# Kernel optimization log

Measured on AMD Instinct MI355X. Metric: run time of the kernel, lower is better.

Reference implementation:

```python
import jax, jax.numpy as jnp
import numpy as np

N_NODES = 100000


def _gcn_norm(edge_index, num_nodes):
    # PyG GCNConv default: add self-loops, symmetric normalization
    row, col = edge_index[0], edge_index[1]
    loop = jnp.arange(num_nodes, dtype=edge_index.dtype)
    row = jnp.concatenate([row, loop])
    col = jnp.concatenate([col, loop])
    ones = jnp.ones(col.shape[0], dtype=jnp.float32)
    deg = jax.ops.segment_sum(ones, col, num_segments=num_nodes)
    dinv = jnp.where(deg > 0, jax.lax.rsqrt(deg), 0.0)
    norm = dinv[row] * dinv[col]  # [E + N]
    return row, col, norm


def _gcn_conv(x, W, b, row, col, norm, num_nodes):
    h = x @ W                               # [N, out] linear transform first
    msg = h[row] * norm[:, None]            # gather + edge-wise scale
    out = jax.ops.segment_sum(msg, col, num_segments=num_nodes)  # scatter-add
    return out + b


def setup_inputs() -> dict:
    key = jax.random.key(0)
    k1, k2, k3, k4 = jax.random.split(key, 4)
    E = 1600000
    x = jax.random.normal(k1, (N_NODES, 128), dtype=jnp.float32)
    edge_index = jax.random.randint(k2, (2, E), 0, N_NODES, dtype=jnp.int64)
    W1 = jax.random.normal(k3, (128, 128), dtype=jnp.float32) * (1.0 / np.sqrt(128))
    b1 = jnp.zeros((128,), dtype=jnp.float32)
    W2 = jax.random.normal(k4, (128, 64), dtype=jnp.float32) * (1.0 / np.sqrt(128))
    b2 = jnp.zeros((64,), dtype=jnp.float32)
    return {"x": x, "edge_index": edge_index, "W1": W1, "b1": b1, "W2": W2, "b2": b2}


def reference(x, edge_index, W1, b1, W2, b2):
    num_nodes = x.shape[0]
    row, col, norm = _gcn_norm(edge_index, num_nodes)
    h = _gcn_conv(x, W1, b1, row, col, norm, num_nodes)
    h = jax.nn.relu(h)
    out = _gcn_conv(h, W2, b2, row, col, norm, num_nodes)
    return out
```

## Files before the change

### kernel.cpp

```cpp
#include <hip/hip_runtime.h>
#include <hip/hip_bf16.h>

typedef unsigned short u16;
typedef short bf16x8 __attribute__((ext_vector_type(8)));
typedef float f32x4 __attribute__((ext_vector_type(4)));

__device__ __forceinline__ float bflo(unsigned u) { return __uint_as_float(u << 16); }
__device__ __forceinline__ float bfhi(unsigned u) { return __uint_as_float(u & 0xffff0000u); }
__device__ __forceinline__ u16 f2bf(float f) {
    unsigned u = __float_as_uint(f);
    return (u16)((u + 0x7fffu + ((u >> 16) & 1u)) >> 16);
}

#define CHUNK 8192
#define BN 512

__global__ __launch_bounds__(256) void hist_kernel(const int* __restrict__ cols,
                                                   unsigned* __restrict__ hist,
                                                   int E, int nbuckets) {
    __shared__ unsigned h[256];
    int t = threadIdx.x, blk = blockIdx.x;
    h[t] = 0;
    __syncthreads();
    int base = blk * CHUNK;
#pragma unroll
    for (int j = 0; j < CHUNK / 256; j++) {
        int i = base + j * 256 + t;
        if (i < E) atomicAdd(&h[((unsigned)cols[i]) >> 9], 1u);
    }
    __syncthreads();
    if (t < nbuckets) hist[blk * nbuckets + t] = h[t];
}

__global__ __launch_bounds__(256) void scanA1_kernel(unsigned* __restrict__ hist,
                                                     unsigned* __restrict__ totals,
                                                     int nblocksA, int nbuckets) {
    __shared__ unsigned s[256];
    int t = threadIdx.x, b = blockIdx.x;
    unsigned val = (t < nblocksA) ? hist[t * nbuckets + b] : 0u;
    s[t] = val;
    __syncthreads();
    for (int off = 1; off < 256; off <<= 1) {
        unsigned v = (t >= off) ? s[t - off] : 0u;
        __syncthreads();
        s[t] += v;
        __syncthreads();
    }
    if (t < nblocksA) hist[t * nbuckets + b] = s[t] - val;
    if (t == 255) totals[b] = s[255];
}

__global__ __launch_bounds__(256) void scanA2_kernel(const unsigned* __restrict__ totals,
                                                     unsigned* __restrict__ bucketbase,
                                                     int nbuckets) {
    __shared__ unsigned s[256];
    int t = threadIdx.x;
    unsigned val = (t < nbuckets) ? totals[t] : 0u;
    s[t] = val;
    __syncthreads();
    for (int off = 1; off < 256; off <<= 1) {
        unsigned v = (t >= off) ? s[t - off] : 0u;
        __syncthreads();
        s[t] += v;
        __syncthreads();
    }
    unsigned ex = s[t] - val;
    if (t < nbuckets) bucketbase[t] = ex;
    if (t == nbuckets - 1) bucketbase[nbuckets] = ex + val;
}

__global__ __launch_bounds__(256) void scatterA_kernel(const int* __restrict__ rows,
                                                       const int* __restrict__ cols,
                                                       const unsigned* __restrict__ hist,
                                                       const unsigned* __restrict__ bucketbase,
                                                       uint2* __restrict__ binned,
                                                       int E, int nbuckets) {
    __shared__ uint2 sp[CHUNK];
    __shared__ unsigned lstart[256];
    __shared__ unsigned lcur[256];
    __shared__ unsigned gbase[256];
    int t = threadIdx.x, blk = blockIdx.x;
    int base = blk * CHUNK;
    int cnt = min(CHUNK, E - base);

    lcur[t] = 0;
    __syncthreads();
    for (int i = t; i < cnt; i += 256)
        atomicAdd(&lcur[((unsigned)cols[base + i]) >> 9], 1u);
    __syncthreads();
    unsigned val = lcur[t];
    lstart[t] = val;
    __syncthreads();
    for (int off = 1; off < 256; off <<= 1) {
        unsigned v = (t >= off) ? lstart[t - off] : 0u;
        __syncthreads();
        lstart[t] += v;
        __syncthreads();
    }
    unsigned ex = lstart[t] - val;
    __syncthreads();
    lstart[t] = ex;
    lcur[t] = ex;
    if (t < nbuckets) gbase[t] = bucketbase[t] + hist[blk * nbuckets + t];
    __syncthreads();
    for (int i = t; i < cnt; i += 256) {
        unsigned c = (unsigned)cols[base + i];
        unsigned r = (unsigned)rows[base + i];
        unsigned pos = atomicAdd(&lcur[c >> 9], 1u);
        sp[pos] = make_uint2(r, c);
    }
    __syncthreads();
    for (int i = t; i < cnt; i += 256) {
        uint2 u = sp[i];
        unsigned g = u.y >> 9;
        binned[gbase[g] + (unsigned)i - lstart[g]] = u;
    }
}

__global__ __launch_bounds__(256) void binB_kernel(const uint2* __restrict__ binned,
                                                   const unsigned* __restrict__ bucketbase,
                                                   int* __restrict__ rowptr,
                                                   float* __restrict__ dinv,
                                                   int* __restrict__ srcidx,
                                                   int N, int E, int nbuckets) {
    __shared__ unsigned cnt[BN + 1];
    __shared__ unsigned sc[BN + 1];
    __shared__ unsigned ps[256];
    int t = threadIdx.x, b = blockIdx.x;
    int lo = b << 9;
    int nn = min(BN, N - lo);
    unsigned s = bucketbase[b], e = bucketbase[b + 1];

    cnt[t] = 0;
    cnt[t + 256] = 0;
    if (t == 0) cnt[BN] = 0;
    __syncthreads();
    for (unsigned i = s + t; i < e; i += 256)
        atomicAdd(&cnt[binned[i].y - lo], 1u);
    __syncthreads();

    unsigned a0 = cnt[2 * t], a1 = cnt[2 * t + 1];
    ps[t] = a0 + a1;
    __syncthreads();
    unsigned val = ps[t];
    for (int off = 1; off < 256; off <<= 1) {
        unsigned v = (t >= off) ? ps[t - off] : 0u;
        __syncthreads();
        ps[t] += v;
        __syncthreads();
    }
    unsigned ex = ps[t] - val;
    sc[2 * t] = ex;
    sc[2 * t + 1] = ex + a0;
    if (t == 255) sc[BN] = ex + val;
    __syncthreads();

    for (int n = t; n < nn; n += 256) {
        unsigned rp = s + sc[n];
        rowptr[lo + n] = (int)rp;
        dinv[lo + n] = rsqrtf((float)(sc[n + 1] - sc[n]) + 1.0f);
        cnt[n] = rp;
    }
    if (b == nbuckets - 1 && t == 0) rowptr[N] = E;
    __syncthreads();

    for (unsigned i = s + t; i < e; i += 256) {
        uint2 u = binned[i];
        unsigned slot = atomicAdd(&cnt[u.y - lo], 1u);
        srcidx[slot] = (int)u.x;
    }
}

__global__ __launch_bounds__(256) void prep_wt(const float* __restrict__ W1,
                                               const float* __restrict__ W2,
                                               u16* __restrict__ WT1,
                                               u16* __restrict__ WT2) {
    int t = blockIdx.x * 256 + threadIdx.x;
    if (t < 128 * 128) {
        int n = t >> 7, k = t & 127;
        WT1[n * 128 + k] = f2bf(W1[k * 128 + n]);
    } else if (t < 128 * 128 + 64 * 128) {
        int i = t - 128 * 128;
        int n = i >> 7, k = i & 127;
        WT2[n * 128 + k] = f2bf(W2[k * 64 + n]);
    }
}

template <int NOUT, bool IN_BF16>
__global__ __launch_bounds__(256) void gemm_mfma(const void* __restrict__ Xv,
                                                 const u16* __restrict__ WT,
                                                 const float* __restrict__ dinv,
                                                 u16* __restrict__ OutH, int nrows) {
    constexpr int LDK = 136;
    __shared__ u16 sX[64 * LDK];
    __shared__ u16 sW[NOUT * LDK];

    const int t = threadIdx.x;
    const int wv = t >> 6, lane = t & 63;
    const int m = lane & 15, q = lane >> 4;
    const int row0 = blockIdx.x * 64;

    for (int idx = t; idx < NOUT * 16; idx += 256) {
        int n = idx >> 4, c = idx & 15;
        *((uint4*)&sW[n * LDK + c * 8]) = ((const uint4*)WT)[idx];
    }
    if (IN_BF16) {
        const u16* X = (const u16*)Xv;
        for (int idx = t; idx < 64 * 16; idx += 256) {
            int r = idx >> 4, c = idx & 15;
            int gr = row0 + r;
            uint4 v = make_uint4(0u, 0u, 0u, 0u);
            if (gr < nrows) v = ((const uint4*)X)[(size_t)gr * 16 + c];
            *((uint4*)&sX[r * LDK + c * 8]) = v;
        }
    } else {
        const float* X = (const float*)Xv;
        for (int idx = t; idx < 64 * 32; idx += 256) {
            int r = idx >> 5, c = idx & 31;
            int gr = row0 + r;
            float4 v = make_float4(0.f, 0.f, 0.f, 0.f);
            if (gr < nrows) v = ((const float4*)X)[(size_t)gr * 32 + c];
            uint2 o;
            o.x = (unsigned)f2bf(v.x) | ((unsigned)f2bf(v.y) << 16);
            o.y = (unsigned)f2bf(v.z) | ((unsigned)f2bf(v.w) << 16);
            *((uint2*)&sX[r * LDK + c * 4]) = o;
        }
    }
    __syncthreads();

    f32x4 acc[NOUT / 16];
#pragma unroll
    for (int i = 0; i < NOUT / 16; i++) acc[i] = (f32x4){0.f, 0.f, 0.f, 0.f};

#pragma unroll
    for (int ks = 0; ks < 4; ks++) {
        const int k0 = ks * 32 + q * 8;
        bf16x8 a = *((const bf16x8*)&sX[(wv * 16 + m) * LDK + k0]);
#pragma unroll
        for (int nt = 0; nt < NOUT / 16; nt++) {
            bf16x8 b = *((const bf16x8*)&sW[(nt * 16 + m) * LDK + k0]);
            acc[nt] = __builtin_amdgcn_mfma_f32_16x16x32_bf16(a, b, acc[nt], 0, 0, 0);
        }
    }

#pragma unroll
    for (int r = 0; r < 4; r++) {
        int gi = row0 + wv * 16 + q * 4 + r;
        if (gi < nrows) {
            float dv = dinv[gi];
#pragma unroll
            for (int nt = 0; nt < NOUT / 16; nt++) {
                OutH[(size_t)gi * NOUT + nt * 16 + m] = f2bf(acc[nt][r] * dv);
            }
        }
    }
}

template <int NH, bool RELU, bool OUT_BF16>
__global__ __launch_bounds__(256) void aggregate(const int* __restrict__ rowptr,
                                                 const int* __restrict__ srcidx,
                                                 const u16* __restrict__ hs,
                                                 const float* __restrict__ dinv,
                                                 const float* __restrict__ bias,
                                                 void* __restrict__ outv, int N) {
    constexpr int WPN = NH / 8;
    int tid = blockIdx.x * 256 + threadIdx.x;
    int node = tid / WPN;
    int fl = tid % WPN;
    if (node >= N) return;

    const uint4* h128 = (const uint4*)hs;
    int start = rowptr[node], end = rowptr[node + 1];

    float a[8];
    {
        uint4 v = h128[(size_t)node * WPN + fl];
        a[0] = bflo(v.x); a[1] = bfhi(v.x); a[2] = bflo(v.y); a[3] = bfhi(v.y);
        a[4] = bflo(v.z); a[5] = bfhi(v.z); a[6] = bflo(v.w); a[7] = bfhi(v.w);
    }

    int nfull = (end - start) >> 3;
    int i = start;
    int r[8], r2[8];
    if (nfull > 0) {
#pragma unroll
        for (int j = 0; j < 8; j++) r[j] = srcidx[i + j];
    }
    for (int b = 0; b < nfull; b++) {
        uint4 u[8];
#pragma unroll
        for (int j = 0; j < 8; j++) u[j] = h128[(size_t)r[j] * WPN + fl];
        if (b + 1 < nfull) {
#pragma unroll
            for (int j = 0; j < 8; j++) r2[j] = srcidx[i + 8 + j];
        }
#pragma unroll
        for (int j = 0; j < 8; j++) {
            a[0] += bflo(u[j].x); a[1] += bfhi(u[j].x);
            a[2] += bflo(u[j].y); a[3] += bfhi(u[j].y);
            a[4] += bflo(u[j].z); a[5] += bfhi(u[j].z);
            a[6] += bflo(u[j].w); a[7] += bfhi(u[j].w);
        }
#pragma unroll
        for (int j = 0; j < 8; j++) r[j] = r2[j];
        i += 8;
    }
    if (i + 4 <= end) {
        int rr[4];
#pragma unroll
        for (int j = 0; j < 4; j++) rr[j] = srcidx[i + j];
        uint4 u[4];
#pragma unroll
        for (int j = 0; j < 4; j++) u[j] = h128[(size_t)rr[j] * WPN + fl];
#pragma unroll
        for (int j = 0; j < 4; j++) {
            a[0] += bflo(u[j].x); a[1] += bfhi(u[j].x);
            a[2] += bflo(u[j].y); a[3] += bfhi(u[j].y);
            a[4] += bflo(u[j].z); a[5] += bfhi(u[j].z);
            a[6] += bflo(u[j].w); a[7] += bfhi(u[j].w);
        }
        i += 4;
    }
    for (; i < end; ++i) {
        uint4 u = h128[(size_t)srcidx[i] * WPN + fl];
        a[0] += bflo(u.x); a[1] += bfhi(u.x);
        a[2] += bflo(u.y); a[3] += bfhi(u.y);
        a[4] += bflo(u.z); a[5] += bfhi(u.z);
        a[6] += bflo(u.w); a[7] += bfhi(u.w);
    }

    float dv = dinv[node];
    float4 bv0 = ((const float4*)bias)[2 * fl];
    float4 bv1 = ((const float4*)bias)[2 * fl + 1];
    float o[8];
    o[0] = dv * a[0] + bv0.x; o[1] = dv * a[1] + bv0.y;
    o[2] = dv * a[2] + bv0.z; o[3] = dv * a[3] + bv0.w;
    o[4] = dv * a[4] + bv1.x; o[5] = dv * a[5] + bv1.y;
    o[6] = dv * a[6] + bv1.z; o[7] = dv * a[7] + bv1.w;
    if (RELU) {
#pragma unroll
        for (int j = 0; j < 8; j++) o[j] = fmaxf(o[j], 0.f);
    }
    if (OUT_BF16) {
        uint4 w;
        w.x = (unsigned)f2bf(o[0]) | ((unsigned)f2bf(o[1]) << 16);
        w.y = (unsigned)f2bf(o[2]) | ((unsigned)f2bf(o[3]) << 16);
        w.z = (unsigned)f2bf(o[4]) | ((unsigned)f2bf(o[5]) << 16);
        w.w = (unsigned)f2bf(o[6]) | ((unsigned)f2bf(o[7]) << 16);
        ((uint4*)outv)[tid] = w;
    } else {
        ((float4*)outv)[2 * tid] = make_float4(o[0], o[1], o[2], o[3]);
        ((float4*)outv)[2 * tid + 1] = make_float4(o[4], o[5], o[6], o[7]);
    }
}

extern "C" void kernel_launch(void* const* d_in, const int* in_sizes, int n_in,
                              void* d_out, int out_size, void* d_ws, size_t ws_size,
                              hipStream_t stream) {
    const float* x  = (const float*)d_in[0];
    const int*   ei = (const int*)d_in[1];
    const float* W1 = (const float*)d_in[2];
    const float* b1 = (const float*)d_in[3];
    const float* W2 = (const float*)d_in[4];
    const float* b2 = (const float*)d_in[5];

    const int N = in_sizes[0] / 128;
    const int E = in_sizes[1] / 2;
    const int* rows = ei;
    const int* cols = ei + E;

    const int nbuckets = (N + BN - 1) / BN;
    const int nblocksA = (E + CHUNK - 1) / CHUNK;

    char* ws = (char*)d_ws;
    size_t off = 0;
    auto alloc = [&](size_t bytes) -> void* {
        void* p = ws + off;
        off = (off + bytes + 1023) & ~(size_t)1023;
        return p;
    };
    unsigned* hist       = (unsigned*)alloc((size_t)nbuckets * nblocksA * 4);
    unsigned* totals     = (unsigned*)alloc(256 * 4);
    unsigned* bucketbase = (unsigned*)alloc((size_t)(nbuckets + 1) * 4);
    uint2*    binned     = (uint2*)alloc((size_t)E * 8);
    int*      rowptr     = (int*)alloc((size_t)(N + 1) * 4);
    float*    dinv       = (float*)alloc((size_t)N * 4);
    int*      srcidx     = (int*)alloc((size_t)E * 4);
    u16*      WT1        = (u16*)alloc((size_t)128 * 128 * 2);
    u16*      WT2        = (u16*)alloc((size_t)64 * 128 * 2);
    u16*      h1s        = (u16*)alloc((size_t)N * 128 * 2);
    u16*      h1b        = (u16*)alloc((size_t)N * 128 * 2);
    u16*      h2s        = h1s;

    hist_kernel<<<nblocksA, 256, 0, stream>>>(cols, hist, E, nbuckets);
    scanA1_kernel<<<nbuckets, 256, 0, stream>>>(hist, totals, nblocksA, nbuckets);
    scanA2_kernel<<<1, 256, 0, stream>>>(totals, bucketbase, nbuckets);
    scatterA_kernel<<<nblocksA, 256, 0, stream>>>(rows, cols, hist, bucketbase, binned, E, nbuckets);
    binB_kernel<<<nbuckets, 256, 0, stream>>>(binned, bucketbase, rowptr, dinv, srcidx, N, E, nbuckets);

    prep_wt<<<96, 256, 0, stream>>>(W1, W2, WT1, WT2);

    gemm_mfma<128, false><<<(N + 63) / 64, 256, 0, stream>>>(x, WT1, dinv, h1s, N);
    aggregate<128, true, true><<<(N * 16 + 255) / 256, 256, 0, stream>>>(
        rowptr, srcidx, h1s, dinv, b1, h1b, N);

    gemm_mfma<64, true><<<(N + 63) / 64, 256, 0, stream>>>(h1b, WT2, dinv, h2s, N);
    aggregate<64, false, false><<<(N * 8 + 255) / 256, 256, 0, stream>>>(
        rowptr, srcidx, h2s, dinv, b2, d_out, N);
}
```

Before: 286.0 us.

## Fuse layer-1 aggregation with layer-2 GEMM and merge weight prep into histogram

The layer-1 gather/aggregate, bias, ReLU and bf16 conversion are fused with the layer-2 MFMA GEMM in a single kernel. Each block aggregates 16 nodes into shared memory and multiplies them by W2 directly, so the N×128 intermediate hidden buffer is never written to or read back from global memory. The weight transpose/convert kernel is folded into extra blocks of the histogram kernel, saving a launch. The trade-off is that each block reloads W2 into shared memory and runs only a small MFMA tile, so per-block overhead goes up.

```diff
diff --git a/kernel.cpp b/kernel.cpp
--- a/kernel.cpp
+++ b/kernel.cpp
@@ -15,11 +15,28 @@
 #define CHUNK 8192
 #define BN 512
 
-__global__ __launch_bounds__(256) void hist_kernel(const int* __restrict__ cols,
-                                                   unsigned* __restrict__ hist,
-                                                   int E, int nbuckets) {
+__global__ __launch_bounds__(256) void hist_prep_kernel(const int* __restrict__ cols,
+                                                        unsigned* __restrict__ hist,
+                                                        int E, int nbuckets, int nblocksA,
+                                                        const float* __restrict__ W1,
+                                                        const float* __restrict__ W2,
+                                                        u16* __restrict__ WT1,
+                                                        u16* __restrict__ WT2) {
+    int blk = blockIdx.x;
+    if (blk >= nblocksA) {
+        int t = (blk - nblocksA) * 256 + threadIdx.x;
+        if (t < 128 * 128) {
+            int n = t >> 7, k = t & 127;
+            WT1[n * 128 + k] = f2bf(W1[k * 128 + n]);
+        } else if (t < 128 * 128 + 64 * 128) {
+            int i = t - 128 * 128;
+            int n = i >> 7, k = i & 127;
+            WT2[n * 128 + k] = f2bf(W2[k * 64 + n]);
+        }
+        return;
+    }
     __shared__ unsigned h[256];
-    int t = threadIdx.x, blk = blockIdx.x;
+    int t = threadIdx.x;
     h[t] = 0;
     __syncthreads();
     int base = blk * CHUNK;
@@ -171,21 +188,6 @@
     }
 }
 
-__global__ __launch_bounds__(256) void prep_wt(const float* __restrict__ W1,
-                                               const float* __restrict__ W2,
-                                               u16* __restrict__ WT1,
-                                               u16* __restrict__ WT2) {
-    int t = blockIdx.x * 256 + threadIdx.x;
-    if (t < 128 * 128) {
-        int n = t >> 7, k = t & 127;
-        WT1[n * 128 + k] = f2bf(W1[k * 128 + n]);
-    } else if (t < 128 * 128 + 64 * 128) {
-        int i = t - 128 * 128;
-        int n = i >> 7, k = i & 127;
-        WT2[n * 128 + k] = f2bf(W2[k * 64 + n]);
-    }
-}
-
 template <int NOUT, bool IN_BF16>
 __global__ __launch_bounds__(256) void gemm_mfma(const void* __restrict__ Xv,
                                                  const u16* __restrict__ WT,
@@ -252,6 +254,128 @@
             for (int nt = 0; nt < NOUT / 16; nt++) {
                 OutH[(size_t)gi * NOUT + nt * 16 + m] = f2bf(acc[nt][r] * dv);
             }
+        }
+    }
+}
+
+__global__ __launch_bounds__(256) void agg1_gemm2(const int* __restrict__ rowptr,
+                                                  const int* __restrict__ srcidx,
+                                                  const u16* __restrict__ hs,
+                                                  const float* __restrict__ dinv,
+                                                  const float* __restrict__ bias,
+                                                  const u16* __restrict__ WT2,
+                                                  u16* __restrict__ h2s, int N) {
+    constexpr int WPN = 16;
+    constexpr int LDK = 136;
+    __shared__ u16 sO[16 * LDK];
+    __shared__ u16 sW[64 * LDK];
+
+    const int t = threadIdx.x;
+    const int node_l = t / WPN;
+    const int fl = t % WPN;
+    const int node = blockIdx.x * 16 + node_l;
+    const bool valid = node < N;
+
+    for (int idx = t; idx < 64 * 16; idx += 256) {
+        int n = idx >> 4, c = idx & 15;
+        *((uint4*)&sW[n * LDK + c * 8]) = ((const uint4*)WT2)[idx];
+    }
+
+    const uint4* h128 = (const uint4*)hs;
+    float a[8];
+#pragma unroll
+    for (int j = 0; j < 8; j++) a[j] = 0.f;
+
+    if (valid) {
+        int start = rowptr[node], end = rowptr[node + 1];
+        {
+            uint4 v = h128[(size_t)node * WPN + fl];
+            a[0] = bflo(v.x); a[1] = bfhi(v.x); a[2] = bflo(v.y); a[3] = bfhi(v.y);
+            a[4] = bflo(v.z); a[5] = bfhi(v.z); a[6] = bflo(v.w); a[7] = bfhi(v.w);
+        }
+        int nfull = (end - start) >> 3;
+        int i = start;
+        int r[8], r2[8];
+        if (nfull > 0) {
+#pragma unroll
+            for (int j = 0; j < 8; j++) r[j] = srcidx[i + j];
+        }
+        for (int b = 0; b < nfull; b++) {
+            uint4 u[8];
+#pragma unroll
+            for (int j = 0; j < 8; j++) u[j] = h128[(size_t)r[j] * WPN + fl];
+            if (b + 1 < nfull) {
+#pragma unroll
+                for (int j = 0; j < 8; j++) r2[j] = srcidx[i + 8 + j];
+            }
+#pragma unroll
+            for (int j = 0; j < 8; j++) {
+                a[0] += bflo(u[j].x); a[1] += bfhi(u[j].x);
+                a[2] += bflo(u[j].y); a[3] += bfhi(u[j].y);
+                a[4] += bflo(u[j].z); a[5] += bfhi(u[j].z);
+                a[6] += bflo(u[j].w); a[7] += bfhi(u[j].w);
+            }
+#pragma unroll
+            for (int j = 0; j < 8; j++) r[j] = r2[j];
+            i += 8;
+        }
+        if (i + 4 <= end) {
+            int rr[4];
+#pragma unroll
+            for (int j = 0; j < 4; j++) rr[j] = srcidx[i + j];
+            uint4 u[4];
+#pragma unroll
+            for (int j = 0; j < 4; j++) u[j] = h128[(size_t)rr[j] * WPN + fl];
+#pragma unroll
+            for (int j = 0; j < 4; j++) {
+                a[0] += bflo(u[j].x); a[1] += bfhi(u[j].x);
+                a[2] += bflo(u[j].y); a[3] += bfhi(u[j].y);
+                a[4] += bflo(u[j].z); a[5] += bfhi(u[j].z);
+                a[6] += bflo(u[j].w); a[7] += bfhi(u[j].w);
+            }
+            i += 4;
+        }
+        for (; i < end; ++i) {
+            uint4 u = h128[(size_t)srcidx[i] * WPN + fl];
+            a[0] += bflo(u.x); a[1] += bfhi(u.x);
+            a[2] += bflo(u.y); a[3] += bfhi(u.y);
+            a[4] += bflo(u.z); a[5] += bfhi(u.z);
+            a[6] += bflo(u.w); a[7] += bfhi(u.w);
+        }
+    }
+
+    float dv = valid ? dinv[node] : 0.f;
+    float4 bv0 = ((const float4*)bias)[2 * fl];
+    float4 bv1 = ((const float4*)bias)[2 * fl + 1];
+    float o[8];
+    o[0] = fmaxf(dv * a[0] + bv0.x, 0.f); o[1] = fmaxf(dv * a[1] + bv0.y, 0.f);
+    o[2] = fmaxf(dv * a[2] + bv0.z, 0.f); o[3] = fmaxf(dv * a[3] + bv0.w, 0.f);
+    o[4] = fmaxf(dv * a[4] + bv1.x, 0.f); o[5] = fmaxf(dv * a[5] + bv1.y, 0.f);
+    o[6] = fmaxf(dv * a[6] + bv1.z, 0.f); o[7] = fmaxf(dv * a[7] + bv1.w, 0.f);
+    uint4 w;
+    w.x = (unsigned)f2bf(o[0]) | ((unsigned)f2bf(o[1]) << 16);
+    w.y = (unsigned)f2bf(o[2]) | ((unsigned)f2bf(o[3]) << 16);
+    w.z = (unsigned)f2bf(o[4]) | ((unsigned)f2bf(o[5]) << 16);
+    w.w = (unsigned)f2bf(o[6]) | ((unsigned)f2bf(o[7]) << 16);
+    *((uint4*)&sO[node_l * LDK + fl * 8]) = w;
+    __syncthreads();
+
+    const int wv = t >> 6, lane = t & 63;
+    const int m = lane & 15, q = lane >> 4;
+    f32x4 acc = (f32x4){0.f, 0.f, 0.f, 0.f};
+#pragma unroll
+    for (int ks = 0; ks < 4; ks++) {
+        const int k0 = ks * 32 + q * 8;
+        bf16x8 af = *((const bf16x8*)&sO[m * LDK + k0]);
+        bf16x8 bf = *((const bf16x8*)&sW[(wv * 16 + m) * LDK + k0]);
+        acc = __builtin_amdgcn_mfma_f32_16x16x32_bf16(af, bf, acc, 0, 0, 0);
+    }
+#pragma unroll
+    for (int r = 0; r < 4; r++) {
+        int gi = blockIdx.x * 16 + q * 4 + r;
+        if (gi < N) {
+            float dvv = dinv[gi];
+            h2s[(size_t)gi * 64 + wv * 16 + m] = f2bf(acc[r] * dvv);
         }
     }
 }
@@ -389,22 +513,19 @@
     u16*      WT1        = (u16*)alloc((size_t)128 * 128 * 2);
     u16*      WT2        = (u16*)alloc((size_t)64 * 128 * 2);
     u16*      h1s        = (u16*)alloc((size_t)N * 128 * 2);
-    u16*      h1b        = (u16*)alloc((size_t)N * 128 * 2);
-    u16*      h2s        = h1s;
-
-    hist_kernel<<<nblocksA, 256, 0, stream>>>(cols, hist, E, nbuckets);
+    u16*      h2s        = (u16*)alloc((size_t)N * 64 * 2);
+
+    hist_prep_kernel<<<nblocksA + 96, 256, 0, stream>>>(cols, hist, E, nbuckets, nblocksA,
+                                                        W1, W2, WT1, WT2);
     scanA1_kernel<<<nbuckets, 256, 0, stream>>>(hist, totals, nblocksA, nbuckets);
     scanA2_kernel<<<1, 256, 0, stream>>>(totals, bucketbase, nbuckets);
     scatterA_kernel<<<nblocksA, 256, 0, stream>>>(rows, cols, hist, bucketbase, binned, E, nbuckets);
     binB_kernel<<<nbuckets, 256, 0, stream>>>(binned, bucketbase, rowptr, dinv, srcidx, N, E, nbuckets);
 
-    prep_wt<<<96, 256, 0, stream>>>(W1, W2, WT1, WT2);
-
     gemm_mfma<128, false><<<(N + 63) / 64, 256, 0, stream>>>(x, WT1, dinv, h1s, N);
-    aggregate<128, true, true><<<(N * 16 + 255) / 256, 256, 0, stream>>>(
-        rowptr, srcidx, h1s, dinv, b1, h1b, N);
-
-    gemm_mfma<64, true><<<(N + 63) / 64, 256, 0, stream>>>(h1b, WT2, dinv, h2s, N);
+
+    agg1_gemm2<<<(N + 15) / 16, 256, 0, stream>>>(rowptr, srcidx, h1s, dinv, b1, WT2, h2s, N);
+
     aggregate<64, false, false><<<(N * 8 + 255) / 256, 256, 0, stream>>>(
         rowptr, srcidx, h2s, dinv, b2, d_out, N);
 }
```

Result: faster. 273.1 us (-4.5%).

## Store hidden features in feature-blocked layout so aggregation gathers fit in cache

Applied to the files above, without the earlier changes.

The GEMM outputs are now written in a feature-sliced layout ([slice][node][16]), and aggregation runs one thread per node per 16-feature slice, with blockIdx picking the slice. Each slice's gather working set is small (100k nodes × 32 bytes, about 3.2 MB), which is meant to raise L2/MALL hit rates for the random neighbour gathers. The weight-transpose prep is merged into the histogram launch to save a kernel launch, and nontemporal loads and stores are used for edge indices and outputs. In exchange, srcidx and rowptr are reread once per slice, and the GEMM stores are scattered across slices.

```diff
diff --git a/kernel.cpp b/kernel.cpp
--- a/kernel.cpp
+++ b/kernel.cpp
@@ -4,6 +4,7 @@
 typedef unsigned short u16;
 typedef short bf16x8 __attribute__((ext_vector_type(8)));
 typedef float f32x4 __attribute__((ext_vector_type(4)));
+typedef unsigned int u32x4 __attribute__((ext_vector_type(4)));
 
 __device__ __forceinline__ float bflo(unsigned u) { return __uint_as_float(u << 16); }
 __device__ __forceinline__ float bfhi(unsigned u) { return __uint_as_float(u & 0xffff0000u); }
@@ -15,11 +16,28 @@
 #define CHUNK 8192
 #define BN 512
 
-__global__ __launch_bounds__(256) void hist_kernel(const int* __restrict__ cols,
-                                                   unsigned* __restrict__ hist,
-                                                   int E, int nbuckets) {
+__global__ __launch_bounds__(256) void hist_prep_kernel(const int* __restrict__ cols,
+                                                        unsigned* __restrict__ hist,
+                                                        int E, int nbuckets, int nblocksA,
+                                                        const float* __restrict__ W1,
+                                                        const float* __restrict__ W2,
+                                                        u16* __restrict__ WT1,
+                                                        u16* __restrict__ WT2) {
+    int blk = blockIdx.x;
+    if (blk >= nblocksA) {
+        int t = (blk - nblocksA) * 256 + threadIdx.x;
+        if (t < 128 * 128) {
+            int n = t >> 7, k = t & 127;
+            WT1[n * 128 + k] = f2bf(W1[k * 128 + n]);
+        } else if (t < 128 * 128 + 64 * 128) {
+            int i = t - 128 * 128;
+            int n = i >> 7, k = i & 127;
+            WT2[n * 128 + k] = f2bf(W2[k * 64 + n]);
+        }
+        return;
+    }
     __shared__ unsigned h[256];
-    int t = threadIdx.x, blk = blockIdx.x;
+    int t = threadIdx.x;
     h[t] = 0;
     __syncthreads();
     int base = blk * CHUNK;
@@ -171,73 +189,45 @@
     }
 }
 
-__global__ __launch_bounds__(256) void prep_wt(const float* __restrict__ W1,
-                                               const float* __restrict__ W2,
-                                               u16* __restrict__ WT1,
-                                               u16* __restrict__ WT2) {
-    int t = blockIdx.x * 256 + threadIdx.x;
-    if (t < 128 * 128) {
-        int n = t >> 7, k = t & 127;
-        WT1[n * 128 + k] = f2bf(W1[k * 128 + n]);
-    } else if (t < 128 * 128 + 64 * 128) {
-        int i = t - 128 * 128;
-        int n = i >> 7, k = i & 127;
-        WT2[n * 128 + k] = f2bf(W2[k * 64 + n]);
-    }
-}
-
-template <int NOUT, bool IN_BF16>
-__global__ __launch_bounds__(256) void gemm_mfma(const void* __restrict__ Xv,
-                                                 const u16* __restrict__ WT,
-                                                 const float* __restrict__ dinv,
-                                                 u16* __restrict__ OutH, int nrows) {
+__global__ __launch_bounds__(256) void gemm1_mfma(const float* __restrict__ X,
+                                                  const u16* __restrict__ WT,
+                                                  const float* __restrict__ dinv,
+                                                  u16* __restrict__ h1t, int N) {
     constexpr int LDK = 136;
     __shared__ u16 sX[64 * LDK];
-    __shared__ u16 sW[NOUT * LDK];
+    __shared__ u16 sW[128 * LDK];
 
     const int t = threadIdx.x;
     const int wv = t >> 6, lane = t & 63;
     const int m = lane & 15, q = lane >> 4;
     const int row0 = blockIdx.x * 64;
 
-    for (int idx = t; idx < NOUT * 16; idx += 256) {
+    for (int idx = t; idx < 128 * 16; idx += 256) {
         int n = idx >> 4, c = idx & 15;
         *((uint4*)&sW[n * LDK + c * 8]) = ((const uint4*)WT)[idx];
     }
-    if (IN_BF16) {
-        const u16* X = (const u16*)Xv;
-        for (int idx = t; idx < 64 * 16; idx += 256) {
-            int r = idx >> 4, c = idx & 15;
-            int gr = row0 + r;
-            uint4 v = make_uint4(0u, 0u, 0u, 0u);
-            if (gr < nrows) v = ((const uint4*)X)[(size_t)gr * 16 + c];
-            *((uint4*)&sX[r * LDK + c * 8]) = v;
-        }
-    } else {
-        const float* X = (const float*)Xv;
-        for (int idx = t; idx < 64 * 32; idx += 256) {
-            int r = idx >> 5, c = idx & 31;
-            int gr = row0 + r;
-            float4 v = make_float4(0.f, 0.f, 0.f, 0.f);
-            if (gr < nrows) v = ((const float4*)X)[(size_t)gr * 32 + c];
-            uint2 o;
-            o.x = (unsigned)f2bf(v.x) | ((unsigned)f2bf(v.y) << 16);
-            o.y = (unsigned)f2bf(v.z) | ((unsigned)f2bf(v.w) << 16);
-            *((uint2*)&sX[r * LDK + c * 4]) = o;
-        }
-    }
-    __syncthreads();
-
-    f32x4 acc[NOUT / 16];
-#pragma unroll
-    for (int i = 0; i < NOUT / 16; i++) acc[i] = (f32x4){0.f, 0.f, 0.f, 0.f};
+    for (int idx = t; idx < 64 * 32; idx += 256) {
+        int r = idx >> 5, c = idx & 31;
+        int gr = row0 + r;
+        float4 v = make_float4(0.f, 0.f, 0.f, 0.f);
+        if (gr < N) v = ((const float4*)X)[(size_t)gr * 32 + c];
+        uint2 o;
+        o.x = (unsigned)f2bf(v.x) | ((unsigned)f2bf(v.y) << 16);
+        o.y = (unsigned)f2bf(v.z) | ((unsigned)f2bf(v.w) << 16);
+        *((uint2*)&sX[r * LDK + c * 4]) = o;
+    }
+    __syncthreads();
+
+    f32x4 acc[8];
+#pragma unroll
+    for (int i = 0; i < 8; i++) acc[i] = (f32x4){0.f, 0.f, 0.f, 0.f};
 
 #pragma unroll
     for (int ks = 0; ks < 4; ks++) {
         const int k0 = ks * 32 + q * 8;
         bf16x8 a = *((const bf16x8*)&sX[(wv * 16 + m) * LDK + k0]);
 #pragma unroll
-        for (int nt = 0; nt < NOUT / 16; nt++) {
+        for (int nt = 0; nt < 8; nt++) {
             bf16x8 b = *((const bf16x8*)&sW[(nt * 16 + m) * LDK + k0]);
             acc[nt] = __builtin_amdgcn_mfma_f32_16x16x32_bf16(a, b, acc[nt], 0, 0, 0);
         }
@@ -246,111 +236,206 @@
 #pragma unroll
     for (int r = 0; r < 4; r++) {
         int gi = row0 + wv * 16 + q * 4 + r;
-        if (gi < nrows) {
+        if (gi < N) {
             float dv = dinv[gi];
 #pragma unroll
-            for (int nt = 0; nt < NOUT / 16; nt++) {
-                OutH[(size_t)gi * NOUT + nt * 16 + m] = f2bf(acc[nt][r] * dv);
+            for (int nt = 0; nt < 8; nt++) {
+                h1t[((size_t)nt * N + gi) * 16 + m] = f2bf(acc[nt][r] * dv);
             }
         }
     }
 }
 
-template <int NH, bool RELU, bool OUT_BF16>
-__global__ __launch_bounds__(256) void aggregate(const int* __restrict__ rowptr,
-                                                 const int* __restrict__ srcidx,
-                                                 const u16* __restrict__ hs,
-                                                 const float* __restrict__ dinv,
-                                                 const float* __restrict__ bias,
-                                                 void* __restrict__ outv, int N) {
-    constexpr int WPN = NH / 8;
-    int tid = blockIdx.x * 256 + threadIdx.x;
-    int node = tid / WPN;
-    int fl = tid % WPN;
+__global__ __launch_bounds__(256) void gemm2_mfma(const u16* __restrict__ h1a,
+                                                  const u16* __restrict__ WT,
+                                                  const float* __restrict__ dinv,
+                                                  u16* __restrict__ h2t, int N) {
+    constexpr int LDK = 136;
+    __shared__ u16 sX[64 * LDK];
+    __shared__ u16 sW[64 * LDK];
+
+    const int t = threadIdx.x;
+    const int wv = t >> 6, lane = t & 63;
+    const int m = lane & 15, q = lane >> 4;
+    const int row0 = blockIdx.x * 64;
+
+    for (int idx = t; idx < 64 * 16; idx += 256) {
+        int n = idx >> 4, c = idx & 15;
+        *((uint4*)&sW[n * LDK + c * 8]) = ((const uint4*)WT)[idx];
+    }
+    for (int idx = t; idx < 1024; idx += 256) {
+        int p = idx & 1, r = (idx >> 1) & 63, s = idx >> 7;
+        int gr = row0 + r;
+        uint4 v = make_uint4(0u, 0u, 0u, 0u);
+        if (gr < N) v = ((const uint4*)h1a)[((size_t)s * N + gr) * 2 + p];
+        *((uint4*)&sX[r * LDK + s * 16 + p * 8]) = v;
+    }
+    __syncthreads();
+
+    f32x4 acc[4];
+#pragma unroll
+    for (int i = 0; i < 4; i++) acc[i] = (f32x4){0.f, 0.f, 0.f, 0.f};
+
+#pragma unroll
+    for (int ks = 0; ks < 4; ks++) {
+        const int k0 = ks * 32 + q * 8;
+        bf16x8 a = *((const bf16x8*)&sX[(wv * 16 + m) * LDK + k0]);
+#pragma unroll
+        for (int nt = 0; nt < 4; nt++) {
+            bf16x8 b = *((const bf16x8*)&sW[(nt * 16 + m) * LDK + k0]);
+            acc[nt] = __builtin_amdgcn_mfma_f32_16x16x32_bf16(a, b, acc[nt], 0, 0, 0);
+        }
+    }
+
+#pragma unroll
+    for (int r = 0; r < 4; r++) {
+        int gi = row0 + wv * 16 + q * 4 + r;
+        if (gi < N) {
+            float dv = dinv[gi];
+#pragma unroll
+            for (int nt = 0; nt < 4; nt++) {
+                h2t[((size_t)nt * N + gi) * 16 + m] = f2bf(acc[nt][r] * dv);
+            }
+        }
+    }
+}
+
+__global__ __launch_bounds__(256) void agg1_kernel(const int* __restrict__ rowptr,
+                                                   const int* __restrict__ srcidx,
+                                                   const u16* __restrict__ h1t,
+                                                   const float* __restrict__ dinv,
+                                                   const float* __restrict__ b1,
+                                                   u16* __restrict__ h1a, int N) {
+    int fb = blockIdx.x & 7;
+    int node = (blockIdx.x >> 3) * 256 + threadIdx.x;
     if (node >= N) return;
-
-    const uint4* h128 = (const uint4*)hs;
+    const uint4* H = (const uint4*)h1t + (size_t)fb * N * 2;
+
+    float a[16];
+    {
+        uint4 u0 = H[node * 2], u1 = H[node * 2 + 1];
+        a[0] = bflo(u0.x); a[1] = bfhi(u0.x); a[2] = bflo(u0.y); a[3] = bfhi(u0.y);
+        a[4] = bflo(u0.z); a[5] = bfhi(u0.z); a[6] = bflo(u0.w); a[7] = bfhi(u0.w);
+        a[8] = bflo(u1.x); a[9] = bfhi(u1.x); a[10] = bflo(u1.y); a[11] = bfhi(u1.y);
+        a[12] = bflo(u1.z); a[13] = bfhi(u1.z); a[14] = bflo(u1.w); a[15] = bfhi(u1.w);
+    }
     int start = rowptr[node], end = rowptr[node + 1];
-
-    float a[8];
+    int nfull = (end - start) >> 2;
+    int i = start;
+    int r[4], r2[4];
+    if (nfull > 0) {
+#pragma unroll
+        for (int j = 0; j < 4; j++) r[j] = __builtin_nontemporal_load(&srcidx[i + j]);
+    }
+    for (int b = 0; b < nfull; b++) {
+        uint4 u0[4], u1[4];
+#pragma unroll
+        for (int j = 0; j < 4; j++) { u0[j] = H[r[j] * 2]; u1[j] = H[r[j] * 2 + 1]; }
+        if (b + 1 < nfull) {
+#pragma unroll
+            for (int j = 0; j < 4; j++) r2[j] = __builtin_nontemporal_load(&srcidx[i + 4 + j]);
+        }
+#pragma unroll
+        for (int j = 0; j < 4; j++) {
+            a[0] += bflo(u0[j].x); a[1] += bfhi(u0[j].x); a[2] += bflo(u0[j].y); a[3] += bfhi(u0[j].y);
+            a[4] += bflo(u0[j].z); a[5] += bfhi(u0[j].z); a[6] += bflo(u0[j].w); a[7] += bfhi(u0[j].w);
+            a[8] += bflo(u1[j].x); a[9] += bfhi(u1[j].x); a[10] += bflo(u1[j].y); a[11] += bfhi(u1[j].y);
+            a[12] += bflo(u1[j].z); a[13] += bfhi(u1[j].z); a[14] += bflo(u1[j].w); a[15] += bfhi(u1[j].w);
+        }
+#pragma unroll
+        for (int j = 0; j < 4; j++) r[j] = r2[j];
+        i += 4;
+    }
+    for (; i < end; ++i) {
+        int rr = __builtin_nontemporal_load(&srcidx[i]);
+        uint4 u0 = H[rr * 2], u1 = H[rr * 2 + 1];
+        a[0] += bflo(u0.x); a[1] += bfhi(u0.x); a[2] += bflo(u0.y); a[3] += bfhi(u0.y);
+        a[4] += bflo(u0.z); a[5] += bfhi(u0.z); a[6] += bflo(u0.w); a[7] += bfhi(u0.w);
+        a[8] += bflo(u1.x); a[9] += bfhi(u1.x); a[10] += bflo(u1.y); a[11] += bfhi(u1.y);
+        a[12] += bflo(u1.z); a[13] += bfhi(u1.z); a[14] += bflo(u1.w); a[15] += bfhi(u1.w);
+    }
+
+    float dv = dinv[node];
+    const float* bp = b1 + fb * 16;
+    u16 pk[16];
+#pragma unroll
+    for (int j = 0; j < 16; j++) pk[j] = f2bf(fmaxf(dv * a[j] + bp[j], 0.f));
+    u32x4 w0, w1;
+    w0[0] = pk[0] | ((unsigned)pk[1] << 16);  w0[1] = pk[2] | ((unsigned)pk[3] << 16);
+    w0[2] = pk[4] | ((unsigned)pk[5] << 16);  w0[3] = pk[6] | ((unsigned)pk[7] << 16);
+    w1[0] = pk[8] | ((unsigned)pk[9] << 16);  w1[1] = pk[10] | ((unsigned)pk[11] << 16);
+    w1[2] = pk[12] | ((unsigned)pk[13] << 16); w1[3] = pk[14] | ((unsigned)pk[15] << 16);
+    u32x4* O = (u32x4*)((uint4*)h1a + (size_t)fb * N * 2);
+    __builtin_nontemporal_store(w0, &O[node * 2]);
+    __builtin_nontemporal_store(w1, &O[node * 2 + 1]);
+}
+
+__global__ __launch_bounds__(256) void agg2_kernel(const int* __restrict__ rowptr,
+                                                   const int* __restrict__ srcidx,
+                                                   const u16* __restrict__ h2t,
+                                                   const float* __restrict__ dinv,
+                                                   const float* __restrict__ b2,
+                                                   float* __restrict__ out, int N) {
+    int fb = blockIdx.x & 3;
+    int node = (blockIdx.x >> 2) * 256 + threadIdx.x;
+    if (node >= N) return;
+    const uint4* H = (const uint4*)h2t + (size_t)fb * N * 2;
+
+    float a[16];
     {
-        uint4 v = h128[(size_t)node * WPN + fl];
-        a[0] = bflo(v.x); a[1] = bfhi(v.x); a[2] = bflo(v.y); a[3] = bfhi(v.y);
-        a[4] = bflo(v.z); a[5] = bfhi(v.z); a[6] = bflo(v.w); a[7] = bfhi(v.w);
-    }
-
-    int nfull = (end - start) >> 3;
+        uint4 u0 = H[node * 2], u1 = H[node * 2 + 1];
+        a[0] = bflo(u0.x); a[1] = bfhi(u0.x); a[2] = bflo(u0.y); a[3] = bfhi(u0.y);
+        a[4] = bflo(u0.z); a[5] = bfhi(u0.z); a[6] = bflo(u0.w); a[7] = bfhi(u0.w);
+        a[8] = bflo(u1.x); a[9] = bfhi(u1.x); a[10] = bflo(u1.y); a[11] = bfhi(u1.y);
+        a[12] = bflo(u1.z); a[13] = bfhi(u1.z); a[14] = bflo(u1.w); a[15] = bfhi(u1.w);
+    }
+    int start = rowptr[node], end = rowptr[node + 1];
+    int nfull = (end - start) >> 2;
     int i = start;
-    int r[8], r2[8];
+    int r[4], r2[4];
     if (nfull > 0) {
 #pragma unroll
-        for (int j = 0; j < 8; j++) r[j] = srcidx[i + j];
+        for (int j = 0; j < 4; j++) r[j] = __builtin_nontemporal_load(&srcidx[i + j]);
     }
     for (int b = 0; b < nfull; b++) {
-        uint4 u[8];
-#pragma unroll
-        for (int j = 0; j < 8; j++) u[j] = h128[(size_t)r[j] * WPN + fl];
+        uint4 u0[4], u1[4];
+#pragma unroll
+        for (int j = 0; j < 4; j++) { u0[j] = H[r[j] * 2]; u1[j] = H[r[j] * 2 + 1]; }
         if (b + 1 < nfull) {
 #pragma unroll
-            for (int j = 0; j < 8; j++) r2[j] = srcidx[i + 8 + j];
-        }
-#pragma unroll
-        for (int j = 0; j < 8; j++) {
-            a[0] += bflo(u[j].x); a[1] += bfhi(u[j].x);
-            a[2] += bflo(u[j].y); a[3] += bfhi(u[j].y);
-            a[4] += bflo(u[j].z); a[5] += bfhi(u[j].z);
-            a[6] += bflo(u[j].w); a[7] += bfhi(u[j].w);
-        }
-#pragma unroll
-        for (int j = 0; j < 8; j++) r[j] = r2[j];
-        i += 8;
-    }
-    if (i + 4 <= end) {
-        int rr[4];
-#pragma unroll
-        for (int j = 0; j < 4; j++) rr[j] = srcidx[i + j];
-        uint4 u[4];
-#pragma unroll
-        for (int j = 0; j < 4; j++) u[j] = h128[(size_t)rr[j] * WPN + fl];
+            for (int j = 0; j < 4; j++) r2[j] = __builtin_nontemporal_load(&srcidx[i + 4 + j]);
+        }
 #pragma unroll
         for (int j = 0; j < 4; j++) {
-            a[0] += bflo(u[j].x); a[1] += bfhi(u[j].x);
-            a[2] += bflo(u[j].y); a[3] += bfhi(u[j].y);
-            a[4] += bflo(u[j].z); a[5] += bfhi(u[j].z);
-            a[6] += bflo(u[j].w); a[7] += bfhi(u[j].w);
-        }
+            a[0] += bflo(u0[j].x); a[1] += bfhi(u0[j].x); a[2] += bflo(u0[j].y); a[3] += bfhi(u0[j].y);
+            a[4] += bflo(u0[j].z); a[5] += bfhi(u0[j].z); a[6] += bflo(u0[j].w); a[7] += bfhi(u0[j].w);
+            a[8] += bflo(u1[j].x); a[9] += bfhi(u1[j].x); a[10] += bflo(u1[j].y); a[11] += bfhi(u1[j].y);
+            a[12] += bflo(u1[j].z); a[13] += bfhi(u1[j].z); a[14] += bflo(u1[j].w); a[15] += bfhi(u1[j].w);
+        }
+#pragma unroll
+        for (int j = 0; j < 4; j++) r[j] = r2[j];
         i += 4;
     }
     for (; i < end; ++i) {
-        uint4 u = h128[(size_t)srcidx[i] * WPN + fl];
-        a[0] += bflo(u.x); a[1] += bfhi(u.x);
-        a[2] += bflo(u.y); a[3] += bfhi(u.y);
-        a[4] += bflo(u.z); a[5] += bfhi(u.z);
-        a[6] += bflo(u.w); a[7] += bfhi(u.w);
+        int rr = __builtin_nontemporal_load(&srcidx[i]);
+        uint4 u0 = H[rr * 2], u1 = H[rr * 2 + 1];
+        a[0] += bflo(u0.x); a[1] += bfhi(u0.x); a[2] += bflo(u0.y); a[3] += bfhi(u0.y);
+        a[4] += bflo(u0.z); a[5] += bfhi(u0.z); a[6] += bflo(u0.w); a[7] += bfhi(u0.w);
+        a[8] += bflo(u1.x); a[9] += bfhi(u1.x); a[10] += bflo(u1.y); a[11] += bfhi(u1.y);
+        a[12] += bflo(u1.z); a[13] += bfhi(u1.z); a[14] += bflo(u1.w); a[15] += bfhi(u1.w);
     }
 
     float dv = dinv[node];
-    float4 bv0 = ((const float4*)bias)[2 * fl];
-    float4 bv1 = ((const float4*)bias)[2 * fl + 1];
-    float o[8];
-    o[0] = dv * a[0] + bv0.x; o[1] = dv * a[1] + bv0.y;
-    o[2] = dv * a[2] + bv0.z; o[3] = dv * a[3] + bv0.w;
-    o[4] = dv * a[4] + bv1.x; o[5] = dv * a[5] + bv1.y;
-    o[6] = dv * a[6] + bv1.z; o[7] = dv * a[7] + bv1.w;
-    if (RELU) {
-#pragma unroll
-        for (int j = 0; j < 8; j++) o[j] = fmaxf(o[j], 0.f);
-    }
-    if (OUT_BF16) {
-        uint4 w;
-        w.x = (unsigned)f2bf(o[0]) | ((unsigned)f2bf(o[1]) << 16);
-        w.y = (unsigned)f2bf(o[2]) | ((unsigned)f2bf(o[3]) << 16);
-        w.z = (unsigned)f2bf(o[4]) | ((unsigned)f2bf(o[5]) << 16);
-        w.w = (unsigned)f2bf(o[6]) | ((unsigned)f2bf(o[7]) << 16);
-        ((uint4*)outv)[tid] = w;
-    } else {
-        ((float4*)outv)[2 * tid] = make_float4(o[0], o[1], o[2], o[3]);
-        ((float4*)outv)[2 * tid + 1] = make_float4(o[4], o[5], o[6], o[7]);
+    const float* bp = b2 + fb * 16;
+    float* op = out + (size_t)node * 64 + fb * 16;
+#pragma unroll
+    for (int j4 = 0; j4 < 4; j4++) {
+        f32x4 o;
+        o[0] = dv * a[j4 * 4 + 0] + bp[j4 * 4 + 0];
+        o[1] = dv * a[j4 * 4 + 1] + bp[j4 * 4 + 1];
+        o[2] = dv * a[j4 * 4 + 2] + bp[j4 * 4 + 2];
+        o[3] = dv * a[j4 * 4 + 3] + bp[j4 * 4 + 3];
+        __builtin_nontemporal_store(o, (f32x4*)(op + j4 * 4));
     }
 }
 
@@ -371,6 +456,7 @@
 
     const int nbuckets = (N + BN - 1) / BN;
     const int nblocksA = (E + CHUNK - 1) / CHUNK;
+    const int ngroups  = (N + 255) / 256;
 
     char* ws = (char*)d_ws;
     size_t off = 0;
@@ -388,23 +474,20 @@
     int*      srcidx     = (int*)alloc((size_t)E * 4);
     u16*      WT1        = (u16*)alloc((size_t)128 * 128 * 2);
     u16*      WT2        = (u16*)alloc((size_t)64 * 128 * 2);
-    u16*      h1s        = (u16*)alloc((size_t)N * 128 * 2);
-    u16*      h1b        = (u16*)alloc((size_t)N * 128 * 2);
-    u16*      h2s        = h1s;
-
-    hist_kernel<<<nblocksA, 256, 0, stream>>>(cols, hist, E, nbuckets);
+    u16*      h1t        = (u16*)alloc((size_t)N * 128 * 2);
+    u16*      h1a        = (u16*)alloc((size_t)N * 128 * 2);
+    u16*      h2t        = (u16*)alloc((size_t)N * 64 * 2);
+
+    hist_prep_kernel<<<nblocksA + 96, 256, 0, stream>>>(cols, hist, E, nbuckets, nblocksA,
+                                                        W1, W2, WT1, WT2);
     scanA1_kernel<<<nbuckets, 256, 0, stream>>>(hist, totals, nblocksA, nbuckets);
     scanA2_kernel<<<1, 256, 0, stream>>>(totals, bucketbase, nbuckets);
     scatterA_kernel<<<nblocksA, 256, 0, stream>>>(rows, cols, hist, bucketbase, binned, E, nbuckets);
     binB_kernel<<<nbuckets, 256, 0, stream>>>(binned, bucketbase, rowptr, dinv, srcidx, N, E, nbuckets);
 
-    prep_wt<<<96, 256, 0, stream>>>(W1, W2, WT1, WT2);
-
-    gemm_mfma<128, false><<<(N + 63) / 64, 256, 0, stream>>>(x, WT1, dinv, h1s, N);
-    aggregate<128, true, true><<<(N * 16 + 255) / 256, 256, 0, stream>>>(
-        rowptr, srcidx, h1s, dinv, b1, h1b, N);
-
-    gemm_mfma<64, true><<<(N + 63) / 64, 256, 0, stream>>>(h1b, WT2, dinv, h2s, N);
-    aggregate<64, false, false><<<(N * 8 + 255) / 256, 256, 0, stream>>>(
-        rowptr, srcidx, h2s, dinv, b2, d_out, N);
-}
+    gemm1_mfma<<<(N + 63) / 64, 256, 0, stream>>>(x, WT1, dinv, h1t, N);
+    agg1_kernel<<<8 * ngroups, 256, 0, stream>>>(rowptr, srcidx, h1t, dinv, b1, h1a, N);
+
+    gemm2_mfma<<<(N + 63) / 64, 256, 0, stream>>>(h1a, WT2, dinv, h2t, N);
+    agg2_kernel<<<4 * ngroups, 256, 0, stream>>>(rowptr, srcidx, h2t, dinv, b2, (float*)d_out, N);
+}
```

After: 403.7 us. +41.2%, slower.
